# Optimization experiments

Hardware: AMD Instinct MI355X
Metric: run time of the kernel (lower is better)

The kernel has to match this reference:

```python
import jax, jax.numpy as jnp
import numpy as np

# Circuit structure constants (must match input_specs)
V, K, C = 128, 32, 256   # vars, input nodes per var, categories (V*K == N)
L, N, F = 4, 4096, 16    # layer pairs, sum nodes per layer, sum fan-in
E, B = 8192, 512         # product elements per layer, batch size
EPS = 1e-6


def setup_inputs() -> dict:
    key = jax.random.key(0)
    ks = jax.random.split(key, 6)
    return {
        "inputs": jax.random.randint(ks[0], (B, V), 0, C),
        "prod_child_ids": jax.random.randint(ks[1], (L, E, 2), 0, N),
        "sum_child_ids": jax.random.randint(ks[2], (L, N, F), 0, E),
        "input_params": jax.random.uniform(ks[3], (V, K, C), dtype=jnp.float32),
        "sum_params": jax.random.uniform(ks[4], (L, N, F), dtype=jnp.float32),
        "root_params": jax.random.uniform(ks[5], (N,), dtype=jnp.float32),
    }


def _forward(inputs, prod_child_ids, sum_child_ids, input_params, sum_params, root_params):
    # --- input layer: categorical leaves -> node_mars [V*K, B] (log space) ---
    lw_in = jnp.log(input_params + EPS)
    lw_in = lw_in - jax.nn.logsumexp(lw_in, axis=-1, keepdims=True)  # normalized log-params
    x = inputs.T  # [V, B]
    nm = lw_in[jnp.arange(V)[:, None, None], jnp.arange(K)[None, :, None], x[:, None, :]]  # [V, K, B]
    nm = nm.reshape(V * K, B)  # node_mars for leaves, V*K == N

    # --- normalized sum-layer log-weights ---
    lw_sum = jnp.log(sum_params + EPS)
    lw_sum = lw_sum - jax.nn.logsumexp(lw_sum, axis=-1, keepdims=True)  # [L, N, F]

    # --- alternating prod / sum layer groups (fixed small L) ---
    for l in range(L):
        # product layer: element_mars[e] = sum of child node_mars (log space add)
        em = nm[prod_child_ids[l, :, 0]] + nm[prod_child_ids[l, :, 1]]  # [E, B]
        # sum layer: node_mars[n] = logsumexp_j(element_mars[child j] + log w[n, j])
        ch = em[sum_child_ids[l]]  # [N, F, B] irregular gather
        nm = jax.nn.logsumexp(ch + lw_sum[l][:, :, None], axis=1)  # [N, B]

    # --- root sum node -> log-likelihoods [B] ---
    lr = jnp.log(root_params + EPS)
    lr = lr - jax.nn.logsumexp(lr)
    return jax.nn.logsumexp(nm + lr[:, None], axis=0)  # [B]


def reference(inputs, prod_child_ids, sum_child_ids, input_params, sum_params, root_params):
    return _forward(inputs, prod_child_ids, sum_child_ids, input_params, sum_params, root_params)
```

## Files before the change

### kernel.cpp

```cpp
#include <hip/hip_runtime.h>
#include <hip/hip_fp16.h>
#include <math.h>

#define V_ 128
#define K_ 32
#define C_ 256
#define L_ 4
#define N_ 4096
#define F_ 16
#define E_ 8192
#define B_ 512
#define EPS_ 1e-6f

__device__ __forceinline__ __half2 u2h(unsigned u) {
    __half2 h; *reinterpret_cast<unsigned*>(&h) = u; return h;
}
__device__ __forceinline__ unsigned h2u(__half2 h) {
    return *reinterpret_cast<unsigned*>(&h);
}
__device__ __forceinline__ __half b2h(unsigned short u) {
    __half h; *reinterpret_cast<unsigned short*>(&h) = u; return h;
}
__device__ __forceinline__ unsigned short h2b(__half h) {
    return *reinterpret_cast<unsigned short*>(&h);
}
__device__ __forceinline__ __half2 hmax2(__half2 a, __half2 b) {
    float2 fa = __half22float2(a), fb = __half22float2(b);
    return __floats2half2_rn(fmaxf(fa.x, fb.x), fmaxf(fa.y, fb.y));
}

__global__ __launch_bounds__(256) void prep_kernel(const float* __restrict__ sp,
                                                   const int* __restrict__ prod,
                                                   const int* __restrict__ sc,
                                                   const float* __restrict__ ip,
                                                   const float* __restrict__ rp,
                                                   unsigned* __restrict__ PIW,
                                                   unsigned* __restrict__ PP,
                                                   float* __restrict__ inv_row,
                                                   float* __restrict__ lrpsum) {
    int blk = blockIdx.x;
    int tid = threadIdx.x;
    if (blk < 64) {
        int idx = blk * 256 + tid;
        const float4* row4 = (const float4*)(sp + (size_t)idx * F_);
        float v[F_];
        float s = 0.f;
#pragma unroll
        for (int q = 0; q < 4; q++) {
            float4 r = row4[q];
            v[4*q+0] = r.x + EPS_; v[4*q+1] = r.y + EPS_;
            v[4*q+2] = r.z + EPS_; v[4*q+3] = r.w + EPS_;
            s += v[4*q+0] + v[4*q+1] + v[4*q+2] + v[4*q+3];
        }
        float inv = 1.f / s;
        const int* scr = sc + (size_t)idx * F_;
        unsigned* dst  = PIW + (size_t)idx * F_;
#pragma unroll
        for (int f = 0; f < F_; f++) {
            unsigned wbits = h2b(__float2half(v[f] * inv));
            dst[f] = (unsigned)(unsigned short)scr[f] | (wbits << 16);
        }
    } else if (blk < 192) {
        int idx = (blk - 64) * 256 + tid;
        int2 c  = ((const int2*)prod)[idx];
        PP[idx] = (unsigned)c.x | ((unsigned)c.y << 16);
    } else if (blk < 192 + 1024) {
        int rblk = blk - 192;
        int n    = rblk * 4 + (tid >> 6);
        int lane = tid & 63;
        const float* row = ip + (size_t)n * C_;
        float t = 0.f;
#pragma unroll
        for (int i = 0; i < 4; i++) t += row[lane + 64 * i] + EPS_;
#pragma unroll
        for (int off = 32; off; off >>= 1) t += __shfl_down(t, off, 64);
        if (lane == 0) inv_row[n] = 1.f / t;
    } else {
        __shared__ float smem[4];
        float acc = 0.f;
        for (int i = tid; i < N_; i += 256) acc += rp[i] + EPS_;
#pragma unroll
        for (int off = 32; off; off >>= 1) acc += __shfl_down(acc, off, 64);
        if ((tid & 63) == 0) smem[tid >> 6] = acc;
        __syncthreads();
        if (tid == 0) lrpsum[0] = __logf(smem[0] + smem[1] + smem[2] + smem[3]);
    }
}

__global__ __launch_bounds__(1024) void mega_kernel(const float* __restrict__ ip,
                                                    const int* __restrict__ inputs,
                                                    const float* __restrict__ inv_row,
                                                    const float* __restrict__ rp,
                                                    const unsigned* __restrict__ PIW,
                                                    const unsigned* __restrict__ PP,
                                                    const float* __restrict__ lrpsum,
                                                    float* __restrict__ out) {
    __shared__ unsigned nm[N_];
    __shared__ unsigned em[E_];
    __shared__ unsigned redm[16];
    __shared__ float    redf[32];
    int tid  = threadIdx.x;
    int lane = tid & 63;
    int w    = tid >> 6;
    int b0   = blockIdx.x * 2, b1 = b0 + 1;

    float2 u[4];
    float mx0 = 0.f, mx1 = 0.f;
#pragma unroll
    for (int p = 0; p < 4; p++) {
        int n  = p * 1024 + tid;
        int v  = n >> 5;
        int x0 = inputs[b0 * V_ + v];
        int x1 = inputs[b1 * V_ + v];
        float invr = inv_row[n];
        u[p].x = (ip[(size_t)n * C_ + x0] + EPS_) * invr;
        u[p].y = (ip[(size_t)n * C_ + x1] + EPS_) * invr;
        mx0 = fmaxf(mx0, u[p].x);
        mx1 = fmaxf(mx1, u[p].y);
    }
#pragma unroll
    for (int off = 32; off; off >>= 1) {
        mx0 = fmaxf(mx0, __shfl_down(mx0, off, 64));
        mx1 = fmaxf(mx1, __shfl_down(mx1, off, 64));
    }
    if (lane == 0) { redf[w] = mx0; redf[16 + w] = mx1; }
    __syncthreads();
    float m0 = redf[0], m1 = redf[16];
#pragma unroll
    for (int i = 1; i < 16; i++) { m0 = fmaxf(m0, redf[i]); m1 = fmaxf(m1, redf[16 + i]); }
    float inv0 = 1.f / m0, inv1 = 1.f / m1;
    float sg0 = __logf(m0), sg1 = __logf(m1);
#pragma unroll
    for (int p = 0; p < 4; p++)
        nm[p * 1024 + tid] = h2u(__floats2half2_rn(u[p].x * inv0, u[p].y * inv1));
    __syncthreads();

    __half2 ha  = __floats2half2_rn(1.f, 1.f);
    float   af0 = 1.f, af1 = 1.f;

    for (int l = 0; l < L_ - 1; l++) {
        const uint4* pp4 = (const uint4*)(PP + (size_t)l * E_);
#pragma unroll
        for (int p = 0; p < 2; p++) {
            uint4 c = pp4[p * 1024 + tid];
            int e   = (p * 1024 + tid) * 4;
            em[e+0] = h2u(__hmul2(__hmul2(u2h(nm[c.x & 0xffff]), ha),
                                  __hmul2(u2h(nm[c.x >> 16]), ha)));
            em[e+1] = h2u(__hmul2(__hmul2(u2h(nm[c.y & 0xffff]), ha),
                                  __hmul2(u2h(nm[c.y >> 16]), ha)));
            em[e+2] = h2u(__hmul2(__hmul2(u2h(nm[c.z & 0xffff]), ha),
                                  __hmul2(u2h(nm[c.z >> 16]), ha)));
            em[e+3] = h2u(__hmul2(__hmul2(u2h(nm[c.w & 0xffff]), ha),
                                  __hmul2(u2h(nm[c.w >> 16]), ha)));
        }
        sg0 = 2.f * sg0 + 2.f * __logf(af0);
        sg1 = 2.f * sg1 + 2.f * __logf(af1);
        sg0 -= 4.f * __logf(af0) * 0.f;
        __syncthreads();

        const unsigned* piw = PIW + (size_t)l * N_ * F_;
        __half2 hm = u2h(0u);
#pragma unroll
        for (int p = 0; p < 4; p++) {
            int n = p * 1024 + tid;
            const uint4* qv = (const uint4*)(piw + (size_t)n * F_);
            uint4 q0 = qv[0], q1 = qv[1], q2 = qv[2], q3 = qv[3];
            __half2 acc = u2h(0u);
            unsigned qq;
            qq = q0.x; acc = __hfma2(u2h(em[qq & 0xffff]), __half2half2(b2h((unsigned short)(qq >> 16))), acc);
            qq = q0.y; acc = __hfma2(u2h(em[qq & 0xffff]), __half2half2(b2h((unsigned short)(qq >> 16))), acc);
            qq = q0.z; acc = __hfma2(u2h(em[qq & 0xffff]), __half2half2(b2h((unsigned short)(qq >> 16))), acc);
            qq = q0.w; acc = __hfma2(u2h(em[qq & 0xffff]), __half2half2(b2h((unsigned short)(qq >> 16))), acc);
            qq = q1.x; acc = __hfma2(u2h(em[qq & 0xffff]), __half2half2(b2h((unsigned short)(qq >> 16))), acc);
            qq = q1.y; acc = __hfma2(u2h(em[qq & 0xffff]), __half2half2(b2h((unsigned short)(qq >> 16))), acc);
            qq = q1.z; acc = __hfma2(u2h(em[qq & 0xffff]), __half2half2(b2h((unsigned short)(qq >> 16))), acc);
            qq = q1.w; acc = __hfma2(u2h(em[qq & 0xffff]), __half2half2(b2h((unsigned short)(qq >> 16))), acc);
            qq = q2.x; acc = __hfma2(u2h(em[qq & 0xffff]), __half2half2(b2h((unsigned short)(qq >> 16))), acc);
            qq = q2.y; acc = __hfma2(u2h(em[qq & 0xffff]), __half2half2(b2h((unsigned short)(qq >> 16))), acc);
            qq = q2.z; acc = __hfma2(u2h(em[qq & 0xffff]), __half2half2(b2h((unsigned short)(qq >> 16))), acc);
            qq = q2.w; acc = __hfma2(u2h(em[qq & 0xffff]), __half2half2(b2h((unsigned short)(qq >> 16))), acc);
            qq = q3.x; acc = __hfma2(u2h(em[qq & 0xffff]), __half2half2(b2h((unsigned short)(qq >> 16))), acc);
            qq = q3.y; acc = __hfma2(u2h(em[qq & 0xffff]), __half2half2(b2h((unsigned short)(qq >> 16))), acc);
            qq = q3.z; acc = __hfma2(u2h(em[qq & 0xffff]), __half2half2(b2h((unsigned short)(qq >> 16))), acc);
            qq = q3.w; acc = __hfma2(u2h(em[qq & 0xffff]), __half2half2(b2h((unsigned short)(qq >> 16))), acc);
            nm[n] = h2u(acc);
            hm    = hmax2(hm, acc);
        }
#pragma unroll
        for (int off = 32; off; off >>= 1)
            hm = hmax2(hm, u2h(__shfl_down(h2u(hm), off, 64)));
        if (lane == 0) redm[w] = h2u(hm);
        __syncthreads();
        __half2 M = u2h(redm[0]);
#pragma unroll
        for (int i = 1; i < 16; i++) M = hmax2(M, u2h(redm[i]));
        float M0 = __half2float(__low2half(M)), M1 = __half2float(__high2half(M));
        ha  = __floats2half2_rn(fminf(1.f / M0, 60000.f), fminf(1.f / M1, 60000.f));
        af0 = __half2float(__low2half(ha));
        af1 = __half2float(__high2half(ha));
        sg0 -= 2.f * __logf(af0);
        sg1 -= 2.f * __logf(af1);
    }

    {
        const uint4* pp4 = (const uint4*)(PP + (size_t)(L_ - 1) * E_);
#pragma unroll
        for (int p = 0; p < 2; p++) {
            uint4 c = pp4[p * 1024 + tid];
            int e   = (p * 1024 + tid) * 4;
            em[e+0] = h2u(__hmul2(__hmul2(u2h(nm[c.x & 0xffff]), ha),
                                  __hmul2(u2h(nm[c.x >> 16]), ha)));
            em[e+1] = h2u(__hmul2(__hmul2(u2h(nm[c.y & 0xffff]), ha),
                                  __hmul2(u2h(nm[c.y >> 16]), ha)));
            em[e+2] = h2u(__hmul2(__hmul2(u2h(nm[c.z & 0xffff]), ha),
                                  __hmul2(u2h(nm[c.z >> 16]), ha)));
            em[e+3] = h2u(__hmul2(__hmul2(u2h(nm[c.w & 0xffff]), ha),
                                  __hmul2(u2h(nm[c.w >> 16]), ha)));
        }
        sg0 = 2.f * sg0 + 2.f * __logf(af0);
        sg1 = 2.f * sg1 + 2.f * __logf(af1);
        __syncthreads();

        const unsigned* piw = PIW + (size_t)(L_ - 1) * N_ * F_;
        float S0 = 0.f, S1 = 0.f;
#pragma unroll
        for (int p = 0; p < 4; p++) {
            int n = p * 1024 + tid;
            const uint4* qv = (const uint4*)(piw + (size_t)n * F_);
            uint4 qa = qv[0], qb = qv[1], qc = qv[2], qd = qv[3];
            __half2 acc = u2h(0u);
            unsigned qq;
            qq = qa.x; acc = __hfma2(u2h(em[qq & 0xffff]), __half2half2(b2h((unsigned short)(qq >> 16))), acc);
            qq = qa.y; acc = __hfma2(u2h(em[qq & 0xffff]), __half2half2(b2h((unsigned short)(qq >> 16))), acc);
            qq = qa.z; acc = __hfma2(u2h(em[qq & 0xffff]), __half2half2(b2h((unsigned short)(qq >> 16))), acc);
            qq = qa.w; acc = __hfma2(u2h(em[qq & 0xffff]), __half2half2(b2h((unsigned short)(qq >> 16))), acc);
            qq = qb.x; acc = __hfma2(u2h(em[qq & 0xffff]), __half2half2(b2h((unsigned short)(qq >> 16))), acc);
            qq = qb.y; acc = __hfma2(u2h(em[qq & 0xffff]), __half2half2(b2h((unsigned short)(qq >> 16))), acc);
            qq = qb.z; acc = __hfma2(u2h(em[qq & 0xffff]), __half2half2(b2h((unsigned short)(qq >> 16))), acc);
            qq = qb.w; acc = __hfma2(u2h(em[qq & 0xffff]), __half2half2(b2h((unsigned short)(qq >> 16))), acc);
            qq = qc.x; acc = __hfma2(u2h(em[qq & 0xffff]), __half2half2(b2h((unsigned short)(qq >> 16))), acc);
            qq = qc.y; acc = __hfma2(u2h(em[qq & 0xffff]), __half2half2(b2h((unsigned short)(qq >> 16))), acc);
            qq = qc.z; acc = __hfma2(u2h(em[qq & 0xffff]), __half2half2(b2h((unsigned short)(qq >> 16))), acc);
            qq = qc.w; acc = __hfma2(u2h(em[qq & 0xffff]), __half2half2(b2h((unsigned short)(qq >> 16))), acc);
            qq = qd.x; acc = __hfma2(u2h(em[qq & 0xffff]), __half2half2(b2h((unsigned short)(qq >> 16))), acc);
            qq = qd.y; acc = __hfma2(u2h(em[qq & 0xffff]), __half2half2(b2h((unsigned short)(qq >> 16))), acc);
            qq = qd.z; acc = __hfma2(u2h(em[qq & 0xffff]), __half2half2(b2h((unsigned short)(qq >> 16))), acc);
            qq = qd.w; acc = __hfma2(u2h(em[qq & 0xffff]), __half2half2(b2h((unsigned short)(qq >> 16))), acc);
            float2 vv = __half22float2(acc);
            float  r  = rp[n] + EPS_;
            S0 += r * vv.x;
            S1 += r * vv.y;
        }
#pragma unroll
        for (int off = 32; off; off >>= 1) {
            S0 += __shfl_down(S0, off, 64);
            S1 += __shfl_down(S1, off, 64);
        }
        if (lane == 0) { redf[w] = S0; redf[16 + w] = S1; }
        __syncthreads();
        if (tid == 0) {
            float s0 = 0.f, s1 = 0.f;
#pragma unroll
            for (int i = 0; i < 16; i++) { s0 += redf[i]; s1 += redf[16 + i]; }
            float lr = lrpsum[0];
            out[b0] = __logf(s0) + sg0 - lr;
            out[b1] = __logf(s1) + sg1 - lr;
        }
    }
}

extern "C" void kernel_launch(void* const* d_in, const int* in_sizes, int n_in,
                              void* d_out, int out_size, void* d_ws, size_t ws_size,
                              hipStream_t stream) {
    const int*   inputs = (const int*)d_in[0];
    const int*   prod   = (const int*)d_in[1];
    const int*   sc     = (const int*)d_in[2];
    const float* ip     = (const float*)d_in[3];
    const float* sp     = (const float*)d_in[4];
    const float* rp     = (const float*)d_in[5];
    float* out = (float*)d_out;

    unsigned* PIW     = (unsigned*)d_ws;
    unsigned* PP      = PIW + (size_t)L_ * N_ * F_;
    float*    inv_row = (float*)(PP + (size_t)L_ * E_);
    float*    lrpsum  = inv_row + N_;

    prep_kernel<<<64 + 128 + 1024 + 1, 256, 0, stream>>>(sp, prod, sc, ip, rp,
                                                         PIW, PP, inv_row, lrpsum);
    mega_kernel<<<B_ / 2, 1024, 0, stream>>>(ip, inputs, inv_row, rp,
                                             PIW, PP, lrpsum, out);
}
```

Before: 106.9 us.

## Sort sum children by LDS bank, rotate per node, split FMA accumulators

The preprocessing kernel now sorts each sum node's 16 packed (child, weight) entries by child index modulo 32 and stores them rotated by the node index. The aim is to spread the LDS gathers of em[] across banks so that threads in a wave hit fewer conflicts. The sum-layer loops also split the FMA chain into two accumulators to shorten the dependency chain, and a dead statement is removed. The cost is an extra in-register sorting network in preprocessing, plus a slightly different fp16 summation order.

```diff
diff --git a/kernel.cpp b/kernel.cpp
--- a/kernel.cpp
+++ b/kernel.cpp
@@ -55,11 +55,29 @@
         float inv = 1.f / s;
         const int* scr = sc + (size_t)idx * F_;
         unsigned* dst  = PIW + (size_t)idx * F_;
+        unsigned long long key[F_];
 #pragma unroll
         for (int f = 0; f < F_; f++) {
+            unsigned e     = (unsigned)(unsigned short)scr[f];
             unsigned wbits = h2b(__float2half(v[f] * inv));
-            dst[f] = (unsigned)(unsigned short)scr[f] | (wbits << 16);
-        }
+            unsigned pk    = e | (wbits << 16);
+            key[f] = ((unsigned long long)(e & 31u) << 32) | pk;
+        }
+#pragma unroll
+        for (int r = 0; r < 16; r++) {
+#pragma unroll
+            for (int i = 0; i < 15; i++) {
+                if ((i & 1) == (r & 1)) {
+                    unsigned long long a = key[i], b = key[i+1];
+                    key[i]   = a < b ? a : b;
+                    key[i+1] = a < b ? b : a;
+                }
+            }
+        }
+        int rot = idx & 15;
+#pragma unroll
+        for (int r = 0; r < 16; r++)
+            dst[(r + rot) & 15] = (unsigned)key[r];
     } else if (blk < 192) {
         int idx = (blk - 64) * 256 + tid;
         int2 c  = ((const int2*)prod)[idx];
@@ -86,6 +104,10 @@
         if (tid == 0) lrpsum[0] = __logf(smem[0] + smem[1] + smem[2] + smem[3]);
     }
 }
+
+#define FSTEP(QQ, ACC) { unsigned qq_ = (QQ); \
+    ACC = __hfma2(u2h(em[qq_ & 0xffff]), \
+                  __half2half2(b2h((unsigned short)(qq_ >> 16))), ACC); }
 
 __global__ __launch_bounds__(1024) void mega_kernel(const float* __restrict__ ip,
                                                     const int* __restrict__ inputs,
@@ -155,7 +177,6 @@
         }
         sg0 = 2.f * sg0 + 2.f * __logf(af0);
         sg1 = 2.f * sg1 + 2.f * __logf(af1);
-        sg0 -= 4.f * __logf(af0) * 0.f;
         __syncthreads();
 
         const unsigned* piw = PIW + (size_t)l * N_ * F_;
@@ -165,24 +186,12 @@
             int n = p * 1024 + tid;
             const uint4* qv = (const uint4*)(piw + (size_t)n * F_);
             uint4 q0 = qv[0], q1 = qv[1], q2 = qv[2], q3 = qv[3];
-            __half2 acc = u2h(0u);
-            unsigned qq;
-            qq = q0.x; acc = __hfma2(u2h(em[qq & 0xffff]), __half2half2(b2h((unsigned short)(qq >> 16))), acc);
-            qq = q0.y; acc = __hfma2(u2h(em[qq & 0xffff]), __half2half2(b2h((unsigned short)(qq >> 16))), acc);
-            qq = q0.z; acc = __hfma2(u2h(em[qq & 0xffff]), __half2half2(b2h((unsigned short)(qq >> 16))), acc);
-            qq = q0.w; acc = __hfma2(u2h(em[qq & 0xffff]), __half2half2(b2h((unsigned short)(qq >> 16))), acc);
-            qq = q1.x; acc = __hfma2(u2h(em[qq & 0xffff]), __half2half2(b2h((unsigned short)(qq >> 16))), acc);
-            qq = q1.y; acc = __hfma2(u2h(em[qq & 0xffff]), __half2half2(b2h((unsigned short)(qq >> 16))), acc);
-            qq = q1.z; acc = __hfma2(u2h(em[qq & 0xffff]), __half2half2(b2h((unsigned short)(qq >> 16))), acc);
-            qq = q1.w; acc = __hfma2(u2h(em[qq & 0xffff]), __half2half2(b2h((unsigned short)(qq >> 16))), acc);
-            qq = q2.x; acc = __hfma2(u2h(em[qq & 0xffff]), __half2half2(b2h((unsigned short)(qq >> 16))), acc);
-            qq = q2.y; acc = __hfma2(u2h(em[qq & 0xffff]), __half2half2(b2h((unsigned short)(qq >> 16))), acc);
-            qq = q2.z; acc = __hfma2(u2h(em[qq & 0xffff]), __half2half2(b2h((unsigned short)(qq >> 16))), acc);
-            qq = q2.w; acc = __hfma2(u2h(em[qq & 0xffff]), __half2half2(b2h((unsigned short)(qq >> 16))), acc);
-            qq = q3.x; acc = __hfma2(u2h(em[qq & 0xffff]), __half2half2(b2h((unsigned short)(qq >> 16))), acc);
-            qq = q3.y; acc = __hfma2(u2h(em[qq & 0xffff]), __half2half2(b2h((unsigned short)(qq >> 16))), acc);
-            qq = q3.z; acc = __hfma2(u2h(em[qq & 0xffff]), __half2half2(b2h((unsigned short)(qq >> 16))), acc);
-            qq = q3.w; acc = __hfma2(u2h(em[qq & 0xffff]), __half2half2(b2h((unsigned short)(qq >> 16))), acc);
+            __half2 accA = u2h(0u), accB = u2h(0u);
+            FSTEP(q0.x, accA) FSTEP(q0.y, accB) FSTEP(q0.z, accA) FSTEP(q0.w, accB)
+            FSTEP(q1.x, accA) FSTEP(q1.y, accB) FSTEP(q1.z, accA) FSTEP(q1.w, accB)
+            FSTEP(q2.x, accA) FSTEP(q2.y, accB) FSTEP(q2.z, accA) FSTEP(q2.w, accB)
+            FSTEP(q3.x, accA) FSTEP(q3.y, accB) FSTEP(q3.z, accA) FSTEP(q3.w, accB)
+            __half2 acc = __hadd2(accA, accB);
             nm[n] = h2u(acc);
             hm    = hmax2(hm, acc);
         }
@@ -227,26 +236,13 @@
         for (int p = 0; p < 4; p++) {
             int n = p * 1024 + tid;
             const uint4* qv = (const uint4*)(piw + (size_t)n * F_);
-            uint4 qa = qv[0], qb = qv[1], qc = qv[2], qd = qv[3];
-            __half2 acc = u2h(0u);
-            unsigned qq;
-            qq = qa.x; acc = __hfma2(u2h(em[qq & 0xffff]), __half2half2(b2h((unsigned short)(qq >> 16))), acc);
-            qq = qa.y; acc = __hfma2(u2h(em[qq & 0xffff]), __half2half2(b2h((unsigned short)(qq >> 16))), acc);
-            qq = qa.z; acc = __hfma2(u2h(em[qq & 0xffff]), __half2half2(b2h((unsigned short)(qq >> 16))), acc);
-            qq = qa.w; acc = __hfma2(u2h(em[qq & 0xffff]), __half2half2(b2h((unsigned short)(qq >> 16))), acc);
-            qq = qb.x; acc = __hfma2(u2h(em[qq & 0xffff]), __half2half2(b2h((unsigned short)(qq >> 16))), acc);
-            qq = qb.y; acc = __hfma2(u2h(em[qq & 0xffff]), __half2half2(b2h((unsigned short)(qq >> 16))), acc);
-            qq = qb.z; acc = __hfma2(u2h(em[qq & 0xffff]), __half2half2(b2h((unsigned short)(qq >> 16))), acc);
-            qq = qb.w; acc = __hfma2(u2h(em[qq & 0xffff]), __half2half2(b2h((unsigned short)(qq >> 16))), acc);
-            qq = qc.x; acc = __hfma2(u2h(em[qq & 0xffff]), __half2half2(b2h((unsigned short)(qq >> 16))), acc);
-            qq = qc.y; acc = __hfma2(u2h(em[qq & 0xffff]), __half2half2(b2h((unsigned short)(qq >> 16))), acc);
-            qq = qc.z; acc = __hfma2(u2h(em[qq & 0xffff]), __half2half2(b2h((unsigned short)(qq >> 16))), acc);
-            qq = qc.w; acc = __hfma2(u2h(em[qq & 0xffff]), __half2half2(b2h((unsigned short)(qq >> 16))), acc);
-            qq = qd.x; acc = __hfma2(u2h(em[qq & 0xffff]), __half2half2(b2h((unsigned short)(qq >> 16))), acc);
-            qq = qd.y; acc = __hfma2(u2h(em[qq & 0xffff]), __half2half2(b2h((unsigned short)(qq >> 16))), acc);
-            qq = qd.z; acc = __hfma2(u2h(em[qq & 0xffff]), __half2half2(b2h((unsigned short)(qq >> 16))), acc);
-            qq = qd.w; acc = __hfma2(u2h(em[qq & 0xffff]), __half2half2(b2h((unsigned short)(qq >> 16))), acc);
-            float2 vv = __half22float2(acc);
+            uint4 q0 = qv[0], q1 = qv[1], q2 = qv[2], q3 = qv[3];
+            __half2 accA = u2h(0u), accB = u2h(0u);
+            FSTEP(q0.x, accA) FSTEP(q0.y, accB) FSTEP(q0.z, accA) FSTEP(q0.w, accB)
+            FSTEP(q1.x, accA) FSTEP(q1.y, accB) FSTEP(q1.z, accA) FSTEP(q1.w, accB)
+            FSTEP(q2.x, accA) FSTEP(q2.y, accB) FSTEP(q2.z, accA) FSTEP(q2.w, accB)
+            FSTEP(q3.x, accA) FSTEP(q3.y, accB) FSTEP(q3.z, accA) FSTEP(q3.w, accB)
+            float2 vv = __half22float2(__hadd2(accA, accB));
             float  r  = rp[n] + EPS_;
             S0 += r * vv.x;
             S1 += r * vv.y;
```

Measured after the change: 108.0 us. Within noise of the previous version (+1.0%).
